# Optimization experiments

Hardware: AMD Instinct MI355X
Metric: run time of the kernel (lower is better)

## Reference

```python
import jax, jax.numpy as jnp
import numpy as np

B, TQ, TV, D = 8, 256, 512, 128
LN_EPS = 1e-3  # Keras LayerNormalization default epsilon


def setup_inputs() -> dict:
    key = jax.random.key(0)
    k1, k2, k3 = jax.random.split(key, 3)
    x = jax.random.normal(k1, (B, TQ, D), dtype=jnp.float32)
    context = jax.random.normal(k2, (B, TV, D), dtype=jnp.float32)
    scale = jax.random.normal(k3, (D,), dtype=jnp.float32)  # AdditiveAttention use_scale vector
    gamma = jnp.ones((D,), dtype=jnp.float32)
    beta = jnp.zeros((D,), dtype=jnp.float32)
    return {"x": x, "context": context, "scale": scale, "gamma": gamma, "beta": beta}


def reference(x, context, scale, gamma, beta):
    # Bahdanau additive attention: scores[b,i,j] = sum_d scale[d]*tanh(x[b,i,d] + context[b,j,d])
    # [B,TQ,TV,D] broadcasted intermediate, contracted over d with the learned scale vector.
    scores = jnp.einsum("bijd,d->bij", jnp.tanh(x[:, :, None, :] + context[:, None, :, :]), scale)
    weights = jax.nn.softmax(scores, axis=-1)          # [B,TQ,TV]
    attn_out = jnp.einsum("bij,bjd->bid", weights, context)  # weighted sum of values (=context)
    # residual add + LayerNorm over last axis
    y = x + attn_out
    mu = jnp.mean(y, axis=-1, keepdims=True)
    var = jnp.mean(jnp.square(y - mu), axis=-1, keepdims=True)
    out = gamma * (y - mu) * jax.lax.rsqrt(var + LN_EPS) + beta
    return out
```

## Files before the change

### kernel.cpp

```cpp
#include <hip/hip_runtime.h>
#include <math.h>

#define BB 8
#define TQ 256
#define TV 512
#define DD 128
#define TI 4
#define LN_EPS 1e-3f

typedef float f4 __attribute__((ext_vector_type(4)));

__global__ __launch_bounds__(256) void prep_kernel(const float* __restrict__ ctx,
                                                   const float* __restrict__ scale,
                                                   float* __restrict__ tc,
                                                   float* __restrict__ tcs) {
    int idx = blockIdx.x * 256 + threadIdx.x;
    const f4* c4 = (const f4*)ctx;
    const f4* s4 = (const f4*)scale;
    f4 c = c4[idx];
    f4 s = s4[idx & 31];
    f4 t, ts;
#pragma unroll
    for (int k = 0; k < 4; ++k) {
        float tv = tanhf(c[k]);
        t[k] = tv;
        ts[k] = tv * s[k];
    }
    ((f4*)tc)[idx] = t;
    ((f4*)tcs)[idx] = ts;
}

__global__ __launch_bounds__(512) void attn_kernel(const float* __restrict__ x,
                                                   const float* __restrict__ ctx,
                                                   const float* __restrict__ scale,
                                                   const float* __restrict__ gamma,
                                                   const float* __restrict__ beta,
                                                   const float* __restrict__ tc,
                                                   const float* __restrict__ tcs,
                                                   float* __restrict__ out) {
    __shared__ float xs[TI * DD];
    __shared__ f4    txT[DD];
    __shared__ f4    AT[DD];
    __shared__ f4    wT[TV];
    __shared__ float red[4 * TI * DD];
    __shared__ f4    mred[8];
    __shared__ f4    sred[8];
    __shared__ float lnred[8][2];

    const int t    = threadIdx.x;
    const int bg   = blockIdx.x;
    const int b    = bg >> 6;
    const int i0   = (bg & 63) * TI;
    const int wv   = t >> 6;
    const int lane = t & 63;

    {
        int r = t >> 7, d = t & 127;
        float v  = x[(size_t)((b * TQ) + i0 + r) * DD + d];
        float sv = scale[d];
        float tv = tanhf(v);
        xs[r * DD + d] = v;
        txT[d][r] = tv;
        AT[d][r]  = sv * tv;
    }
    __syncthreads();

    float acc[TI] = {0.f, 0.f, 0.f, 0.f};
    {
        const f4* tcp  = (const f4*)(tc  + (size_t)(b * TV + t) * DD);
        const f4* tcsp = (const f4*)(tcs + (size_t)(b * TV + t) * DD);
#pragma unroll 4
        for (int d4 = 0; d4 < DD / 4; ++d4) {
            f4 c  = tcp[d4];
            f4 cs = tcsp[d4];
#pragma unroll
            for (int k = 0; k < 4; ++k) {
                int d = d4 * 4 + k;
                f4 tx4 = txT[d];
                f4 A4  = AT[d];
#pragma unroll
                for (int r = 0; r < TI; ++r) {
                    float num = A4[r] + cs[k];
                    float den = fmaf(tx4[r], c[k], 1.0f);
                    acc[r] = fmaf(num, __builtin_amdgcn_rcpf(den), acc[r]);
                }
            }
        }
    }

    f4 m;
#pragma unroll
    for (int r = 0; r < TI; ++r) m[r] = acc[r];
#pragma unroll
    for (int off = 32; off > 0; off >>= 1) {
#pragma unroll
        for (int r = 0; r < TI; ++r) m[r] = fmaxf(m[r], __shfl_xor(m[r], off));
    }
    if (lane == 0) mred[wv] = m;
    __syncthreads();
    f4 M = mred[0];
#pragma unroll
    for (int w = 1; w < 8; ++w) {
        f4 o = mred[w];
#pragma unroll
        for (int r = 0; r < TI; ++r) M[r] = fmaxf(M[r], o[r]);
    }
    f4 e;
#pragma unroll
    for (int r = 0; r < TI; ++r) e[r] = __expf(acc[r] - M[r]);
    f4 s = e;
#pragma unroll
    for (int off = 32; off > 0; off >>= 1) {
#pragma unroll
        for (int r = 0; r < TI; ++r) s[r] += __shfl_xor(s[r], off);
    }
    if (lane == 0) sred[wv] = s;
    __syncthreads();
    f4 S = sred[0];
#pragma unroll
    for (int w = 1; w < 8; ++w) {
        f4 o = sred[w];
#pragma unroll
        for (int r = 0; r < TI; ++r) S[r] += o[r];
    }
    f4 w4;
#pragma unroll
    for (int r = 0; r < TI; ++r) w4[r] = e[r] * __builtin_amdgcn_rcpf(S[r]);
    wT[t] = w4;
    __syncthreads();

    {
        const int g = t >> 7;
        const int d = t & 127;
        const float* cp = ctx + (size_t)(b * TV + g * 128) * DD + d;
        f4 p = {0.f, 0.f, 0.f, 0.f};
#pragma unroll 4
        for (int jj = 0; jj < 128; ++jj) {
            f4 wj = wT[g * 128 + jj];
            float cv = cp[(size_t)jj * DD];
#pragma unroll
            for (int r = 0; r < TI; ++r) p[r] = fmaf(wj[r], cv, p[r]);
        }
#pragma unroll
        for (int r = 0; r < TI; ++r) red[(g * TI + r) * DD + d] = p[r];
    }
    __syncthreads();

    {
        const int r = t >> 7;
        const int d = t & 127;
        float attn = red[(0 * TI + r) * DD + d] + red[(1 * TI + r) * DD + d] +
                     red[(2 * TI + r) * DD + d] + red[(3 * TI + r) * DD + d];
        float y = xs[r * DD + d] + attn;
        float s1 = y, s2 = y * y;
#pragma unroll
        for (int off = 32; off > 0; off >>= 1) {
            s1 += __shfl_xor(s1, off);
            s2 += __shfl_xor(s2, off);
        }
        if (lane == 0) { lnred[wv][0] = s1; lnred[wv][1] = s2; }
        __syncthreads();
        float S1 = lnred[2 * r][0] + lnred[2 * r + 1][0];
        float S2 = lnred[2 * r][1] + lnred[2 * r + 1][1];
        float mu  = S1 * (1.0f / 128.0f);
        float var = S2 * (1.0f / 128.0f) - mu * mu;
        float inv = rsqrtf(var + LN_EPS);
        out[(size_t)((b * TQ) + i0 + r) * DD + d] = gamma[d] * (y - mu) * inv + beta[d];
    }
}

extern "C" void kernel_launch(void* const* d_in, const int* in_sizes, int n_in,
                              void* d_out, int out_size, void* d_ws, size_t ws_size,
                              hipStream_t stream) {
    const float* x     = (const float*)d_in[0];
    const float* ctx   = (const float*)d_in[1];
    const float* scale = (const float*)d_in[2];
    const float* gamma = (const float*)d_in[3];
    const float* beta  = (const float*)d_in[4];
    float* out = (float*)d_out;

    float* tc  = (float*)d_ws;
    float* tcs = tc + (size_t)BB * TV * DD;

    prep_kernel<<<(BB * TV * DD / 4) / 256, 256, 0, stream>>>(ctx, scale, tc, tcs);
    attn_kernel<<<(BB * TQ) / TI, 512, 0, stream>>>(x, ctx, scale, gamma, beta, tc, tcs, out);
}
```

Measured before the change: 109.8 us.

## Rewrite tanh scores as exp-product reciprocal and split D across 1024 threads

```diff
diff --git a/kernel.cpp b/kernel.cpp
--- a/kernel.cpp
+++ b/kernel.cpp
@@ -6,97 +6,93 @@
 #define TV 512
 #define DD 128
 #define TI 4
+#define NT 1024
 #define LN_EPS 1e-3f
 
 typedef float f4 __attribute__((ext_vector_type(4)));
 
 __global__ __launch_bounds__(256) void prep_kernel(const float* __restrict__ ctx,
-                                                   const float* __restrict__ scale,
-                                                   float* __restrict__ tc,
-                                                   float* __restrict__ tcs) {
+                                                   float* __restrict__ F) {
     int idx = blockIdx.x * 256 + threadIdx.x;
-    const f4* c4 = (const f4*)ctx;
-    const f4* s4 = (const f4*)scale;
-    f4 c = c4[idx];
-    f4 s = s4[idx & 31];
-    f4 t, ts;
+    f4 c = ((const f4*)ctx)[idx];
+    f4 r;
 #pragma unroll
-    for (int k = 0; k < 4; ++k) {
-        float tv = tanhf(c[k]);
-        t[k] = tv;
-        ts[k] = tv * s[k];
-    }
-    ((f4*)tc)[idx] = t;
-    ((f4*)tcs)[idx] = ts;
+    for (int k = 0; k < 4; ++k) r[k] = __expf(2.0f * c[k]);
+    ((f4*)F)[idx] = r;
 }
 
-__global__ __launch_bounds__(512) void attn_kernel(const float* __restrict__ x,
-                                                   const float* __restrict__ ctx,
-                                                   const float* __restrict__ scale,
-                                                   const float* __restrict__ gamma,
-                                                   const float* __restrict__ beta,
-                                                   const float* __restrict__ tc,
-                                                   const float* __restrict__ tcs,
-                                                   float* __restrict__ out) {
+__global__ __launch_bounds__(NT, 8) void attn_kernel(const float* __restrict__ x,
+                                                     const float* __restrict__ ctx,
+                                                     const float* __restrict__ scale,
+                                                     const float* __restrict__ gamma,
+                                                     const float* __restrict__ beta,
+                                                     const float* __restrict__ F,
+                                                     float* __restrict__ out) {
     __shared__ float xs[TI * DD];
-    __shared__ f4    txT[DD];
-    __shared__ f4    AT[DD];
+    __shared__ f4    txE[DD];
+    __shared__ float s2n[DD];
+    __shared__ f4    pacc[TV];
     __shared__ f4    wT[TV];
-    __shared__ float red[4 * TI * DD];
+    __shared__ float red[8][TI][DD];
     __shared__ f4    mred[8];
     __shared__ f4    sred[8];
     __shared__ float lnred[8][2];
 
-    const int t    = threadIdx.x;
-    const int bg   = blockIdx.x;
-    const int b    = bg >> 6;
-    const int i0   = (bg & 63) * TI;
+    const int t  = threadIdx.x;
+    const int bg = blockIdx.x;
+    const int wg   = (bg & 7) * 64 + (bg >> 3);
+    const int b    = wg >> 6;
+    const int i0   = (wg & 63) * TI;
     const int wv   = t >> 6;
     const int lane = t & 63;
 
-    {
+    if (t < TI * DD) {
         int r = t >> 7, d = t & 127;
-        float v  = x[(size_t)((b * TQ) + i0 + r) * DD + d];
-        float sv = scale[d];
-        float tv = tanhf(v);
-        xs[r * DD + d] = v;
-        txT[d][r] = tv;
-        AT[d][r]  = sv * tv;
+        float v = x[(size_t)(b * TQ + i0 + r) * DD + d];
+        xs[t] = v;
+        txE[d][r] = __expf(2.0f * v);
     }
+    if (t >= 512 && t < 512 + DD) s2n[t - 512] = -2.0f * scale[t - 512];
     __syncthreads();
 
-    float acc[TI] = {0.f, 0.f, 0.f, 0.f};
+    const int j = t & 511;
+    const int h = t >> 9;
+    f4 acc = {0.f, 0.f, 0.f, 0.f};
     {
-        const f4* tcp  = (const f4*)(tc  + (size_t)(b * TV + t) * DD);
-        const f4* tcsp = (const f4*)(tcs + (size_t)(b * TV + t) * DD);
-#pragma unroll 4
-        for (int d4 = 0; d4 < DD / 4; ++d4) {
-            f4 c  = tcp[d4];
-            f4 cs = tcsp[d4];
+        const f4* Fp = (const f4*)(F + (size_t)(b * TV + j) * DD + h * 64);
+#pragma unroll 2
+        for (int d4 = 0; d4 < 16; ++d4) {
+            f4 Fv = Fp[d4];
 #pragma unroll
             for (int k = 0; k < 4; ++k) {
-                int d = d4 * 4 + k;
-                f4 tx4 = txT[d];
-                f4 A4  = AT[d];
+                const int d = h * 64 + d4 * 4 + k;
+                f4 E = txE[d];
+                float sn = s2n[d];
+                f4 den, u;
 #pragma unroll
-                for (int r = 0; r < TI; ++r) {
-                    float num = A4[r] + cs[k];
-                    float den = fmaf(tx4[r], c[k], 1.0f);
-                    acc[r] = fmaf(num, __builtin_amdgcn_rcpf(den), acc[r]);
-                }
+                for (int r = 0; r < TI; ++r) den[r] = fmaf(E[r], Fv[k], 1.0f);
+#pragma unroll
+                for (int r = 0; r < TI; ++r) u[r] = __builtin_amdgcn_rcpf(den[r]);
+#pragma unroll
+                for (int r = 0; r < TI; ++r) acc[r] = fmaf(sn, u[r], acc[r]);
             }
         }
     }
+    if (h == 1) pacc[j] = acc;
+    __syncthreads();
+    if (h == 0) {
+        f4 o = pacc[j];
+#pragma unroll
+        for (int r = 0; r < TI; ++r) acc[r] += o[r];
+    }
 
-    f4 m;
-#pragma unroll
-    for (int r = 0; r < TI; ++r) m[r] = acc[r];
+    f4 m = acc;
 #pragma unroll
     for (int off = 32; off > 0; off >>= 1) {
 #pragma unroll
         for (int r = 0; r < TI; ++r) m[r] = fmaxf(m[r], __shfl_xor(m[r], off));
     }
-    if (lane == 0) mred[wv] = m;
+    if (lane == 0 && wv < 8) mred[wv] = m;
     __syncthreads();
     f4 M = mred[0];
 #pragma unroll
@@ -114,7 +110,7 @@
 #pragma unroll
         for (int r = 0; r < TI; ++r) s[r] += __shfl_xor(s[r], off);
     }
-    if (lane == 0) sred[wv] = s;
+    if (lane == 0 && wv < 8) sred[wv] = s;
     __syncthreads();
     f4 S = sred[0];
 #pragma unroll
@@ -123,49 +119,57 @@
 #pragma unroll
         for (int r = 0; r < TI; ++r) S[r] += o[r];
     }
-    f4 w4;
+    if (h == 0) {
+        f4 w4;
 #pragma unroll
-    for (int r = 0; r < TI; ++r) w4[r] = e[r] * __builtin_amdgcn_rcpf(S[r]);
-    wT[t] = w4;
+        for (int r = 0; r < TI; ++r) w4[r] = e[r] * __builtin_amdgcn_rcpf(S[r]);
+        wT[j] = w4;
+    }
     __syncthreads();
 
     {
         const int g = t >> 7;
         const int d = t & 127;
-        const float* cp = ctx + (size_t)(b * TV + g * 128) * DD + d;
+        const float* cp = ctx + (size_t)(b * TV + g * 64) * DD + d;
         f4 p = {0.f, 0.f, 0.f, 0.f};
 #pragma unroll 4
-        for (int jj = 0; jj < 128; ++jj) {
-            f4 wj = wT[g * 128 + jj];
+        for (int jj = 0; jj < 64; ++jj) {
+            f4 wj = wT[g * 64 + jj];
             float cv = cp[(size_t)jj * DD];
 #pragma unroll
             for (int r = 0; r < TI; ++r) p[r] = fmaf(wj[r], cv, p[r]);
         }
 #pragma unroll
-        for (int r = 0; r < TI; ++r) red[(g * TI + r) * DD + d] = p[r];
+        for (int r = 0; r < TI; ++r) red[g][r][d] = p[r];
     }
     __syncthreads();
 
     {
         const int r = t >> 7;
         const int d = t & 127;
-        float attn = red[(0 * TI + r) * DD + d] + red[(1 * TI + r) * DD + d] +
-                     red[(2 * TI + r) * DD + d] + red[(3 * TI + r) * DD + d];
-        float y = xs[r * DD + d] + attn;
+        float y = 0.f;
+        if (t < 512) {
+            float attn = 0.f;
+#pragma unroll
+            for (int g = 0; g < 8; ++g) attn += red[g][r][d];
+            y = xs[r * DD + d] + attn;
+        }
         float s1 = y, s2 = y * y;
 #pragma unroll
         for (int off = 32; off > 0; off >>= 1) {
             s1 += __shfl_xor(s1, off);
             s2 += __shfl_xor(s2, off);
         }
-        if (lane == 0) { lnred[wv][0] = s1; lnred[wv][1] = s2; }
+        if (lane == 0 && wv < 8) { lnred[wv][0] = s1; lnred[wv][1] = s2; }
         __syncthreads();
-        float S1 = lnred[2 * r][0] + lnred[2 * r + 1][0];
-        float S2 = lnred[2 * r][1] + lnred[2 * r + 1][1];
-        float mu  = S1 * (1.0f / 128.0f);
-        float var = S2 * (1.0f / 128.0f) - mu * mu;
-        float inv = rsqrtf(var + LN_EPS);
-        out[(size_t)((b * TQ) + i0 + r) * DD + d] = gamma[d] * (y - mu) * inv + beta[d];
+        if (t < 512) {
+            float S1 = lnred[2 * r][0] + lnred[2 * r + 1][0];
+            float S2 = lnred[2 * r][1] + lnred[2 * r + 1][1];
+            float mu  = S1 * (1.0f / 128.0f);
+            float var = S2 * (1.0f / 128.0f) - mu * mu;
+            float inv = rsqrtf(var + LN_EPS);
+            out[(size_t)(b * TQ + i0 + r) * DD + d] = gamma[d] * (y - mu) * inv + beta[d];
+        }
     }
 }
 
@@ -179,9 +183,8 @@
     const float* beta  = (const float*)d_in[4];
     float* out = (float*)d_out;
 
-    float* tc  = (float*)d_ws;
-    float* tcs = tc + (size_t)BB * TV * DD;
+    float* F = (float*)d_ws;
 
-    prep_kernel<<<(BB * TV * DD / 4) / 256, 256, 0, stream>>>(ctx, scale, tc, tcs);
-    attn_kernel<<<(BB * TQ) / TI, 512, 0, stream>>>(x, ctx, scale, gamma, beta, tc, tcs, out);
+    prep_kernel<<<(BB * TV * DD / 4) / 256, 256, 0, stream>>>(ctx, F);
+    attn_kernel<<<(BB * TQ) / TI, NT, 0, stream>>>(x, ctx, scale, gamma, beta, F, out);
 }
```

Measured after the change: 90.91 us. 1.21x faster.
